# Performance work log

Measured on AMD Instinct MI355X. Metric: run time of the kernel, lower is better.

Reference implementation:

```python
import jax, jax.numpy as jnp
import numpy as np

B, SQ, SV = 2, 2048, 2048
DV, DQ, DK, DO, H = 1024, 1280, 1024, 1024, 16
DHK, DHO = DK // H, DO // H


def setup_inputs() -> dict:
    key = jax.random.key(0)
    ks = jax.random.split(key, 8)
    pre_value_key = jax.random.normal(ks[0], (B, SV, DV), jnp.float32)
    pre_query = jax.random.normal(ks[1], (B, SQ, DQ), jnp.float32)
    value_key_masks = (jax.random.uniform(ks[2], (B, SV)) < 0.9).astype(jnp.float32)
    value_key_counts = jnp.maximum(value_key_masks.sum(-1), 1.0)
    s = 0.02
    Wq = jax.random.normal(ks[3], (DQ, DK), jnp.float32) * s
    bq = jnp.zeros((DK,), jnp.float32)
    Wk = jax.random.normal(ks[4], (DV, DK), jnp.float32) * s
    bk = jnp.zeros((DK,), jnp.float32)
    Wv = jax.random.normal(ks[5], (DV, DO), jnp.float32) * s
    bv = jnp.zeros((DO,), jnp.float32)
    overall_gain = jnp.ones((1, H, 1, 1), jnp.float32)
    overall_bias = jnp.full((1, H, 1, 1), -10.0, jnp.float32)
    return dict(pre_value_key=pre_value_key, pre_query=pre_query,
                value_key_masks=value_key_masks, value_key_counts=value_key_counts,
                Wq=Wq, bq=bq, Wk=Wk, bk=bk, Wv=Wv, bv=bv,
                overall_gain=overall_gain, overall_bias=overall_bias)


def _heads(x, h):
    # (B, S, D) -> (B, h, S, D//h)
    b, s, d = x.shape
    return x.reshape(b, s, h, d // h).transpose(0, 2, 1, 3)


def reference(pre_value_key, pre_query, value_key_masks, value_key_counts,
              Wq, bq, Wk, bk, Wv, bv, overall_gain, overall_bias):
    q = _heads(pre_query @ Wq + bq, H)        # (B,H,SQ,DHK)
    k = _heads(pre_value_key @ Wk + bk, H)    # (B,H,SV,DHK)
    v = _heads(pre_value_key @ Wv + bv, H)    # (B,H,SV,DHO)

    scores = jnp.einsum('bhqd,bhkd->bhqk', q, k) / jnp.sqrt(jnp.float32(DHK))

    mask = value_key_masks  # (B,SV), 0/1 float
    # pooled-score sigmoid gate (cross-attn branch)
    pooled = (scores * mask[:, None, None, :]).sum(-1, keepdims=True)
    pooled = pooled / value_key_counts[:, None, None, None]
    overall_weight = jax.nn.sigmoid(pooled * overall_gain + overall_bias)  # (B,H,SQ,1)

    add_mask = jnp.where(mask == 0, -jnp.inf, 0.0).astype(scores.dtype)
    sm = jax.nn.softmax(scores + add_mask[:, None, None, :], axis=-1)
    h = jnp.einsum('bhqk,bhkd->bhqd', sm, v)  # (B,H,SQ,DHO)

    pq_split = _heads(pre_query[:, :, :DO], H)  # (B,H,SQ,DHO)
    out = pq_split * (1.0 - overall_weight) + h * overall_weight
    out = out.transpose(0, 2, 1, 3).reshape(B, SQ, DO)
    out = jnp.concatenate([out, pre_query[:, :, DO:]], axis=-1)  # (B,SQ,DQ)
    return out
```

## Files before the change

### kernel.cpp

```cpp
#include <hip/hip_runtime.h>

typedef __attribute__((ext_vector_type(8))) __bf16 bf16x8;
typedef __attribute__((ext_vector_type(4))) float f32x4;
typedef __attribute__((ext_vector_type(16))) float f32x16;
typedef __attribute__((ext_vector_type(4))) unsigned short us4;
typedef __attribute__((ext_vector_type(4))) unsigned int u32x4;
typedef __attribute__((address_space(3))) void* as3vp;
typedef const __attribute__((address_space(1))) void* as1vp;

#define GLOAD_LDS16(g, l) __builtin_amdgcn_global_load_lds((as1vp)(g), (as3vp)(l), 16, 0, 0)

#if __has_builtin(__builtin_amdgcn_exp2f)
#define EXP2(x) __builtin_amdgcn_exp2f(x)
#else
#define EXP2(x) __expf((x) * 0.6931471805599453f)
#endif

__device__ __forceinline__ unsigned short f2bf(float f) {
  unsigned u = __builtin_bit_cast(unsigned, f);
  u += 0x7FFFu + ((u >> 16) & 1u);
  return (unsigned short)(u >> 16);
}
__device__ __forceinline__ float bf2f(unsigned short u) {
  return __builtin_bit_cast(float, (unsigned)u << 16);
}
__device__ __forceinline__ unsigned int pkbf(float a, float b) {
  unsigned int r;
  asm("v_cvt_pk_bf16_f32 %0, %1, %2" : "=v"(r) : "v"(a), "v"(b));
  return r;
}

__global__ void prep_all(const float* __restrict__ pre_q, const float* __restrict__ pre_vk,
                         const float* __restrict__ Wq, const float* __restrict__ Wk,
                         const float* __restrict__ Wv, const float* __restrict__ vmask,
                         unsigned short* __restrict__ pq_bf, unsigned short* __restrict__ pv_bf,
                         unsigned short* __restrict__ WqT, unsigned short* __restrict__ WkT,
                         unsigned short* __restrict__ WvT, float* __restrict__ addm,
                         float* __restrict__ km, float* __restrict__ out) {
  __shared__ float tsh[32][33];
  const int bid = blockIdx.x, tid = threadIdx.x;
  if (bid < 5120) {
    const int i = bid * 256 + tid;
    float4 v = ((const float4*)pre_q)[i];
    us4 o;
    o.x = f2bf(v.x); o.y = f2bf(v.y); o.z = f2bf(v.z); o.w = f2bf(v.w);
    ((us4*)pq_bf)[i] = o;
    if ((i % 320) >= 256) ((float4*)out)[i] = v;
  } else if (bid < 9216) {
    const int i = (bid - 5120) * 256 + tid;
    float4 v = ((const float4*)pre_vk)[i];
    us4 o;
    o.x = f2bf(v.x); o.y = f2bf(v.y); o.z = f2bf(v.z); o.w = f2bf(v.w);
    ((us4*)pv_bf)[i] = o;
  } else if (bid < 13056) {
    const int tb = bid - 9216;
    const int z = tb / 1280, rem = tb % 1280;
    const int x = rem & 31, y = rem >> 5;
    const int K = (z == 0) ? 1280 : 1024;
    if (y * 32 >= K) return;
    const float* W = (z == 0) ? Wq : ((z == 1) ? Wk : Wv);
    unsigned short* WT = (z == 0) ? WqT : ((z == 1) ? WkT : WvT);
    const int tx = tid & 31, ty = tid >> 5;
    const int n0 = x * 32, k0 = y * 32;
#pragma unroll
    for (int i = 0; i < 32; i += 8)
      tsh[ty + i][tx] = W[(size_t)(k0 + ty + i) * 1024 + n0 + tx];
    __syncthreads();
#pragma unroll
    for (int i = 0; i < 32; i += 8)
      WT[(size_t)(n0 + ty + i) * K + k0 + tx] = f2bf(tsh[tx][ty + i]);
  } else {
    const int i = (bid - 13056) * 256 + tid;
    addm[i] = (vmask[i] != 0.f) ? 0.f : -1e30f;
    if (i < 2048) km[i] = 0.f;
  }
}

__global__ __launch_bounds__(256, 3)
void gemm_all(const unsigned short* __restrict__ Aq,
              const unsigned short* __restrict__ Akv,
              const unsigned short* __restrict__ WqT,
              const unsigned short* __restrict__ WkT,
              const unsigned short* __restrict__ WvT,
              const float* __restrict__ bq,
              const float* __restrict__ bk,
              const float* __restrict__ bv,
              const float* __restrict__ vmask,
              unsigned short* __restrict__ Qout,
              unsigned short* __restrict__ Kout,
              unsigned short* __restrict__ VFout,
              float* __restrict__ km) {
  __shared__ unsigned short sAB[2][2][128 * 32];
  const int fblk = blockIdx.x;
  const int z = fblk % 3;
  const int rest = fblk / 3;
  const int bx = rest & 31, by = rest >> 5;
  const int KDIM = (z == 0) ? 1280 : 1024;
  const unsigned short* A = (z == 0) ? Aq : Akv;
  const unsigned short* Bt = (z == 0) ? WqT : ((z == 1) ? WkT : WvT);

  const int tid = threadIdx.x, lane = tid & 63, w = tid >> 6;
  const int l15 = lane & 15, lhi = lane >> 4;
  const int wm = w >> 1, wn = w & 1;
  const int row0 = bx * 128, col0 = by * 128;

  const f32x4 zv = {0.f, 0.f, 0.f, 0.f};
  f32x4 acc[4][4];
#pragma unroll
  for (int m = 0; m < 4; ++m)
#pragma unroll
    for (int n = 0; n < 4; ++n) acc[m][n] = zv;

  auto stage = [&](int buf, int kt) {
#pragma unroll
    for (int i = 0; i < 2; ++i) {
      const int c = i * 256 + tid;
      const int r = c >> 2, kc = ((c & 3) ^ (r & 3)) * 8;
      GLOAD_LDS16(A + (size_t)(row0 + r) * KDIM + kt + kc, &sAB[buf][0][0] + c * 8);
      GLOAD_LDS16(Bt + (size_t)(col0 + r) * KDIM + kt + kc, &sAB[buf][1][0] + c * 8);
    }
  };

  const int NT = KDIM / 32;
  stage(0, 0);
  __syncthreads();
  int cur = 0;
  for (int t = 0; t < NT; ++t) {
    if (t + 1 < NT) stage(cur ^ 1, (t + 1) * 32);
    const unsigned short* sAb = &sAB[cur][0][0];
    const unsigned short* sBb = &sAB[cur][1][0];
    const int koS = ((lhi ^ (l15 & 3)) * 8);
    bf16x8 af[4], bfr[4];
#pragma unroll
    for (int m = 0; m < 4; ++m) af[m] = *(const bf16x8*)(sAb + (wm * 64 + m * 16 + l15) * 32 + koS);
#pragma unroll
    for (int n = 0; n < 4; ++n) bfr[n] = *(const bf16x8*)(sBb + (wn * 64 + n * 16 + l15) * 32 + koS);
#pragma unroll
    for (int m = 0; m < 4; ++m)
#pragma unroll
      for (int n = 0; n < 4; ++n)
        acc[m][n] = __builtin_amdgcn_mfma_f32_16x16x32_bf16(af[m], bfr[n], acc[m][n], 0, 0, 0);
    __syncthreads();
    cur ^= 1;
  }

  if (z == 0) {
#pragma unroll
    for (int n = 0; n < 4; ++n) {
      const int gc = col0 + wn * 64 + n * 16 + l15;
      const float bb = bq[gc];
#pragma unroll
      for (int m = 0; m < 4; ++m) {
        const int gr0 = row0 + wm * 64 + m * 16 + lhi * 4;
#pragma unroll
        for (int r = 0; r < 4; ++r)
          Qout[(size_t)(gr0 + r) * 1024 + gc] = f2bf((acc[m][n][r] + bb) * 0.18033688f);
      }
    }
  } else if (z == 1) {
    const int b_ = row0 >> 11;
    const float* maskb = vmask + b_ * 2048;
    f32x4 mv[4];
#pragma unroll
    for (int m = 0; m < 4; ++m)
      mv[m] = *(const f32x4*)(maskb + (row0 & 2047) + wm * 64 + m * 16 + lhi * 4);
#pragma unroll
    for (int n = 0; n < 4; ++n) {
      const int gc = col0 + wn * 64 + n * 16 + l15;
      const float bb = bk[gc];
      float s = 0.f;
#pragma unroll
      for (int m = 0; m < 4; ++m) {
        const int gr0 = row0 + wm * 64 + m * 16 + lhi * 4;
#pragma unroll
        for (int r = 0; r < 4; ++r) {
          const float val = acc[m][n][r] + bb;
          Kout[(size_t)(gr0 + r) * 1024 + gc] = f2bf(val);
          s = fmaf(mv[m][r], val, s);
        }
      }
      s += __shfl_xor(s, 16, 64);
      s += __shfl_xor(s, 32, 64);
      if (lhi == 0) atomicAdd(&km[(b_ * 16 + (gc >> 6)) * 64 + (gc & 63)], s);
    }
  } else {
    __syncthreads();
    unsigned* tb = (unsigned*)&sAB[0][0][0];
#pragma unroll
    for (int n = 0; n < 4; ++n) {
      const int gcL = wn * 64 + n * 16 + l15;
      const float bb = bv[col0 + gcL];
#pragma unroll
      for (int m = 0; m < 4; ++m) {
#pragma unroll
        for (int k = 0; k < 2; ++k) {
          const int grPair = wm * 32 + m * 8 + lhi * 2 + k;
          const int W = (grPair & 3) | ((((grPair >> 2) ^ gcL) & 15) << 2);
          tb[gcL * 64 + W] = pkbf(acc[m][n][2 * k] + bb, acc[m][n][2 * k + 1] + bb);
        }
      }
    }
    __syncthreads();
    const int b_ = row0 >> 11;
#pragma unroll
    for (int it = 0; it < 8; ++it) {
      const int c = it * 256 + tid;
      const int gcL = (c & 63) + ((c >> 10) << 6);
      const int u = (c >> 6) & 15;
      const int W4 = (u ^ gcL) & 15;
      u32x4 o = *(const u32x4*)(tb + gcL * 64 + W4 * 4);
      const int kv0 = (row0 & 2047) + u * 8;
      const int ch = col0 + gcL;
      const int hh2 = ch >> 6, d = ch & 63;
      const int t2 = kv0 >> 6, ks2 = (kv0 >> 4) & 3, h5v = (kv0 >> 3) & 1;
      const size_t off = ((size_t)(b_ * 16 + hh2) << 17) +
                         (size_t)(((t2 * 4 + ks2) * 2 + (d >> 5)) * 64 + h5v * 32 + (d & 31)) * 8;
      *(u32x4*)(VFout + off) = o;
    }
  }
}

__global__ __launch_bounds__(256, 2)
void attn_fused(const unsigned short* __restrict__ Q,
                const unsigned short* __restrict__ Kb,
                const unsigned short* __restrict__ VF,
                const float* __restrict__ addm_g,
                const float* __restrict__ km,
                const float* __restrict__ counts,
                const float* __restrict__ gain,
                const float* __restrict__ gbias,
                const float* __restrict__ pq,
                float* __restrict__ out) {
  __shared__ __align__(16) char smem[32768];
  unsigned short* sK = (unsigned short*)smem;
  float* saddm = (float*)(smem + 16384);
  float* sOT = (float*)smem;

  const int tid = threadIdx.x, lane = tid & 63, w = tid >> 6;
  const int l31 = lane & 31, h5 = lane >> 5;
  const int f = blockIdx.x;
  const int qt = (f >> 3) & 15;
  const int bh = (f & 7) + 8 * (f >> 7);
  const int b = bh >> 4, hh = bh & 15;
  const int q0 = qt * 128;

  GLOAD_LDS16(addm_g + b * 2048 + tid * 4, (char*)saddm + tid * 16);
  GLOAD_LDS16(addm_g + b * 2048 + 1024 + tid * 4, (char*)saddm + 4096 + tid * 16);

  bf16x8 qf[4];
  {
    const unsigned short* qp = Q + (size_t)(b * 2048 + q0 + w * 32 + l31) * 1024 + hh * 64 + h5 * 8;
#pragma unroll
    for (int ks = 0; ks < 4; ++ks) qf[ks] = *(const bf16x8*)(qp + ks * 16);
  }

  float pl_s = 0.f;
  {
    const float* kmp = km + (b * 16 + hh) * 64 + h5 * 8;
#pragma unroll
    for (int ks = 0; ks < 4; ++ks) {
      f32x4 ka = *(const f32x4*)(kmp + ks * 16);
      f32x4 kb4 = *(const f32x4*)(kmp + ks * 16 + 4);
#pragma unroll
      for (int j = 0; j < 4; ++j)
        pl_s += (float)qf[ks][j] * ka[j] + (float)qf[ks][j + 4] * kb4[j];
    }
    float ta = pl_s, tb = pl_s;
    asm("v_permlane32_swap_b32 %0, %1" : "+v"(ta), "+v"(tb));
    pl_s = ta + tb;
  }

  const unsigned short* Kbase = Kb + (size_t)(b * 2048) * 1024 + hh * 64;
  const unsigned short* VFb = VF + ((size_t)bh << 17) + lane * 8;

  f32x16 o0, o1, l_vec;
#pragma unroll
  for (int r = 0; r < 16; ++r) { o0[r] = 0.f; o1[r] = 0.f; l_vec[r] = 0.f; }
  float m_ = -1e30f;

  auto stageK = [&](int buf, int kv) {
#pragma unroll
    for (int i = 0; i < 2; ++i) {
      const int c = i * 256 + tid;
      const int r = c >> 3, sl = (c & 7) ^ (r & 7);
      GLOAD_LDS16(Kbase + (size_t)(kv + r) * 1024 + sl * 8, (char*)sK + buf * 8192 + c * 16);
    }
  };

  bf16x8 vf[8];
  auto ldV = [&](int t) {
    const unsigned short* p = VFb + (size_t)t * 4096;
#pragma unroll
    for (int i = 0; i < 8; ++i) vf[i] = *(const bf16x8*)(p + i * 512);
  };

  stageK(0, 0);
  __syncthreads();
  int cur = 0;

  for (int t = 0; t < 32; ++t) {
    if (t < 31) stageK(cur ^ 1, (t + 1) * 64);
    ldV(t);
    const char* sKc = (const char*)sK + cur * 8192;

    f32x16 s0, s1;
#pragma unroll
    for (int g = 0; g < 4; ++g) {
      f32x4 a0 = *(const f32x4*)(saddm + t * 64 + g * 8 + h5 * 4);
      f32x4 a1 = *(const f32x4*)(saddm + t * 64 + 32 + g * 8 + h5 * 4);
#pragma unroll
      for (int j = 0; j < 4; ++j) { s0[g * 4 + j] = a0[j]; s1[g * 4 + j] = a1[j]; }
    }

#pragma unroll
    for (int ks = 0; ks < 4; ++ks) {
      const int sl = (((ks * 2 + h5) ^ (l31 & 7)) * 16);
      bf16x8 k0 = *(const bf16x8*)(sKc + l31 * 128 + sl);
      bf16x8 k1 = *(const bf16x8*)(sKc + (32 + l31) * 128 + sl);
      s0 = __builtin_amdgcn_mfma_f32_32x32x16_bf16(k0, qf[ks], s0, 0, 0, 0);
      s1 = __builtin_amdgcn_mfma_f32_32x32x16_bf16(k1, qf[ks], s1, 0, 0, 0);
    }

    f32x16 mx;
#pragma unroll
    for (int r = 0; r < 16; ++r) mx[r] = fmaxf(s0[r], s1[r]);
    float t8[8];
#pragma unroll
    for (int r = 0; r < 8; ++r) t8[r] = fmaxf(mx[r], mx[r + 8]);
    float tp = fmaxf(fmaxf(fmaxf(t8[0], t8[1]), fmaxf(t8[2], t8[3])),
                     fmaxf(fmaxf(t8[4], t8[5]), fmaxf(t8[6], t8[7])));
    {
      float ta = tp, tb = tp;
      asm("v_permlane32_swap_b32 %0, %1" : "+v"(ta), "+v"(tb));
      tp = fmaxf(ta, tb);
    }
    if (__any(tp > m_ + 11.0f)) {
      const float mnew = fmaxf(m_, tp);
      const float corr = EXP2(m_ - mnew);
      m_ = mnew;
      l_vec *= corr; o0 *= corr; o1 *= corr;
    }

    f32x16 p0, p1;
#pragma unroll
    for (int r = 0; r < 16; ++r) p0[r] = EXP2(s0[r] - m_);
#pragma unroll
    for (int r = 0; r < 16; ++r) p1[r] = EXP2(s1[r] - m_);
    l_vec += p0; l_vec += p1;

    bf16x8 pfs[4];
    {
      unsigned x0 = pkbf(p0[0], p0[1]), y0 = pkbf(p0[2], p0[3]);
      unsigned z0 = pkbf(p0[4], p0[5]), w0 = pkbf(p0[6], p0[7]);
      asm("v_permlane32_swap_b32 %0, %1" : "+v"(x0), "+v"(z0));
      asm("v_permlane32_swap_b32 %0, %1" : "+v"(y0), "+v"(w0));
      u32x4 f0 = {x0, y0, z0, w0};
      pfs[0] = __builtin_bit_cast(bf16x8, f0);
      unsigned x1 = pkbf(p0[8], p0[9]), y1 = pkbf(p0[10], p0[11]);
      unsigned z1 = pkbf(p0[12], p0[13]), w1 = pkbf(p0[14], p0[15]);
      asm("v_permlane32_swap_b32 %0, %1" : "+v"(x1), "+v"(z1));
      asm("v_permlane32_swap_b32 %0, %1" : "+v"(y1), "+v"(w1));
      u32x4 f1 = {x1, y1, z1, w1};
      pfs[1] = __builtin_bit_cast(bf16x8, f1);
      unsigned x2 = pkbf(p1[0], p1[1]), y2 = pkbf(p1[2], p1[3]);
      unsigned z2 = pkbf(p1[4], p1[5]), w2 = pkbf(p1[6], p1[7]);
      asm("v_permlane32_swap_b32 %0, %1" : "+v"(x2), "+v"(z2));
      asm("v_permlane32_swap_b32 %0, %1" : "+v"(y2), "+v"(w2));
      u32x4 f2 = {x2, y2, z2, w2};
      pfs[2] = __builtin_bit_cast(bf16x8, f2);
      unsigned x3 = pkbf(p1[8], p1[9]), y3 = pkbf(p1[10], p1[11]);
      unsigned z3 = pkbf(p1[12], p1[13]), w3 = pkbf(p1[14], p1[15]);
      asm("v_permlane32_swap_b32 %0, %1" : "+v"(x3), "+v"(z3));
      asm("v_permlane32_swap_b32 %0, %1" : "+v"(y3), "+v"(w3));
      u32x4 f3 = {x3, y3, z3, w3};
      pfs[3] = __builtin_bit_cast(bf16x8, f3);
    }

#pragma unroll
    for (int ks = 0; ks < 4; ++ks) {
      o0 = __builtin_amdgcn_mfma_f32_32x32x16_bf16(vf[ks * 2], pfs[ks], o0, 0, 0, 0);
      o1 = __builtin_amdgcn_mfma_f32_32x32x16_bf16(vf[ks * 2 + 1], pfs[ks], o1, 0, 0, 0);
    }
    __syncthreads();
    cur ^= 1;
  }

  float l_s;
  {
    float a[8];
#pragma unroll
    for (int r = 0; r < 8; ++r) a[r] = l_vec[r] + l_vec[r + 8];
    l_s = ((a[0] + a[1]) + (a[2] + a[3])) + ((a[4] + a[5]) + (a[6] + a[7]));
    float ta = l_s, tb = l_s;
    asm("v_permlane32_swap_b32 %0, %1" : "+v"(ta), "+v"(tb));
    l_s = ta + tb;
  }
  const float po = pl_s * 0.6931471805599453f / counts[b];
  const float wgv = 1.f / (1.f + __expf(-(po * gain[hh] + gbias[hh])));
  const float invl = 1.f / l_s;

  __syncthreads();
  float* myOT = sOT + w * 2048;
#pragma unroll
  for (int r = 0; r < 16; ++r) {
    const int d0 = (r & 3) + 8 * (r >> 2) + 4 * h5;
    myOT[d0 * 32 + (l31 ^ (d0 & 31))] = o0[r] * invl;
    const int d1 = d0 + 32;
    myOT[d1 * 32 + (l31 ^ (d1 & 31))] = o1[r] * invl;
  }
  __syncthreads();
  const size_t rowbase = (size_t)(b * 2048 + q0 + w * 32) * 1280 + hh * 64 + lane;
  const float* pqrow = pq + rowbase;
  float* outrow = out + rowbase;
#pragma unroll 4
  for (int i = 0; i < 32; ++i) {
    const float hval = myOT[lane * 32 + (i ^ (lane & 31))];
    const float wgrow = __shfl(wgv, i, 64);
    const float pv = pqrow[(size_t)i * 1280];
    outrow[(size_t)i * 1280] = fmaf(hval - pv, wgrow, pv);
  }
}

extern "C" void kernel_launch(void* const* d_in, const int* in_sizes, int n_in,
                              void* d_out, int out_size, void* d_ws, size_t ws_size,
                              hipStream_t stream) {
  const float* pre_vk = (const float*)d_in[0];
  const float* pre_q  = (const float*)d_in[1];
  const float* vmask  = (const float*)d_in[2];
  const float* vcnt   = (const float*)d_in[3];
  const float* Wq = (const float*)d_in[4];
  const float* bq = (const float*)d_in[5];
  const float* Wk = (const float*)d_in[6];
  const float* bk = (const float*)d_in[7];
  const float* Wv = (const float*)d_in[8];
  const float* bv = (const float*)d_in[9];
  const float* gain  = (const float*)d_in[10];
  const float* gbias = (const float*)d_in[11];
  float* out = (float*)d_out;

  char* ws = (char*)d_ws;
  unsigned short* pq_bf = (unsigned short*)(ws);
  unsigned short* pv_bf = (unsigned short*)(ws + 10485760);
  unsigned short* WqT   = (unsigned short*)(ws + 18874368);
  unsigned short* WkT   = (unsigned short*)(ws + 21495808);
  unsigned short* WvT   = (unsigned short*)(ws + 23592960);
  unsigned short* Qb    = (unsigned short*)(ws + 25690112);
  unsigned short* Kbb   = (unsigned short*)(ws + 34078720);
  unsigned short* VFb   = (unsigned short*)(ws + 42467328);
  float*          kmb   = (float*)(ws + 50855936);
  float*          addm  = (float*)(ws + 50864128);

  prep_all<<<13072, 256, 0, stream>>>(pre_q, pre_vk, Wq, Wk, Wv, vmask,
                                      pq_bf, pv_bf, WqT, WkT, WvT, addm, kmb, out);
  gemm_all<<<768, 256, 0, stream>>>(pq_bf, pv_bf, WqT, WkT, WvT, bq, bk, bv, vmask,
                                    Qb, Kbb, VFb, kmb);
  attn_fused<<<512, 256, 0, stream>>>(Qb, Kbb, VFb, addm, kmb, vcnt, gain, gbias, pre_q, out);
}
```

Measured before the change: 106.9 us.

## Process two KV tiles per iteration with split softmax states and MFMA priority

The attention loop now handles 128 keys per iteration as two independent 64-key streams, each with its own running max, denominator and output accumulators, merged once at the end. K staging doubles to 16KB per buffer, so fewer barriers run, and the two independent chains give the scheduler more MFMA/softmax work to interleave. s_setprio is raised around MFMA sections. The cost is much higher register pressure from the duplicated accumulators and V fragments, which could spill or hurt occupancy under launch_bounds(256,2), plus more LDS.

```diff
diff --git a/kernel.cpp b/kernel.cpp
--- a/kernel.cpp
+++ b/kernel.cpp
@@ -231,9 +231,9 @@
                 const float* __restrict__ gbias,
                 const float* __restrict__ pq,
                 float* __restrict__ out) {
-  __shared__ __align__(16) char smem[32768];
+  __shared__ __align__(16) char smem[40960];
   unsigned short* sK = (unsigned short*)smem;
-  float* saddm = (float*)(smem + 16384);
+  float* saddm = (float*)(smem + 32768);
   float* sOT = (float*)smem;
 
   const int tid = threadIdx.x, lane = tid & 63, w = tid >> 6;
@@ -273,140 +273,203 @@
   const unsigned short* Kbase = Kb + (size_t)(b * 2048) * 1024 + hh * 64;
   const unsigned short* VFb = VF + ((size_t)bh << 17) + lane * 8;
 
-  f32x16 o0, o1, l_vec;
-#pragma unroll
-  for (int r = 0; r < 16; ++r) { o0[r] = 0.f; o1[r] = 0.f; l_vec[r] = 0.f; }
-  float m_ = -1e30f;
+  f32x16 oA0, oA1, oB0, oB1, lA, lB;
+#pragma unroll
+  for (int r = 0; r < 16; ++r) {
+    oA0[r] = 0.f; oA1[r] = 0.f; oB0[r] = 0.f; oB1[r] = 0.f;
+    lA[r] = 0.f; lB[r] = 0.f;
+  }
+  float mA = -1e30f, mB = -1e30f;
 
   auto stageK = [&](int buf, int kv) {
 #pragma unroll
-    for (int i = 0; i < 2; ++i) {
+    for (int i = 0; i < 4; ++i) {
       const int c = i * 256 + tid;
       const int r = c >> 3, sl = (c & 7) ^ (r & 7);
-      GLOAD_LDS16(Kbase + (size_t)(kv + r) * 1024 + sl * 8, (char*)sK + buf * 8192 + c * 16);
+      GLOAD_LDS16(Kbase + (size_t)(kv + r) * 1024 + sl * 8, (char*)sK + buf * 16384 + c * 16);
     }
   };
 
-  bf16x8 vf[8];
-  auto ldV = [&](int t) {
+  auto ldV = [&](int t, bf16x8 (&vv)[8]) {
     const unsigned short* p = VFb + (size_t)t * 4096;
 #pragma unroll
-    for (int i = 0; i < 8; ++i) vf[i] = *(const bf16x8*)(p + i * 512);
+    for (int i = 0; i < 8; ++i) vv[i] = *(const bf16x8*)(p + i * 512);
+  };
+
+  auto mkpfs = [&](const f32x16& p0, const f32x16& p1, bf16x8 (&pfs)[4]) {
+    unsigned x0 = pkbf(p0[0], p0[1]), y0 = pkbf(p0[2], p0[3]);
+    unsigned z0 = pkbf(p0[4], p0[5]), w0 = pkbf(p0[6], p0[7]);
+    asm("v_permlane32_swap_b32 %0, %1" : "+v"(x0), "+v"(z0));
+    asm("v_permlane32_swap_b32 %0, %1" : "+v"(y0), "+v"(w0));
+    u32x4 f0 = {x0, y0, z0, w0};
+    pfs[0] = __builtin_bit_cast(bf16x8, f0);
+    unsigned x1 = pkbf(p0[8], p0[9]), y1 = pkbf(p0[10], p0[11]);
+    unsigned z1 = pkbf(p0[12], p0[13]), w1 = pkbf(p0[14], p0[15]);
+    asm("v_permlane32_swap_b32 %0, %1" : "+v"(x1), "+v"(z1));
+    asm("v_permlane32_swap_b32 %0, %1" : "+v"(y1), "+v"(w1));
+    u32x4 f1 = {x1, y1, z1, w1};
+    pfs[1] = __builtin_bit_cast(bf16x8, f1);
+    unsigned x2 = pkbf(p1[0], p1[1]), y2 = pkbf(p1[2], p1[3]);
+    unsigned z2 = pkbf(p1[4], p1[5]), w2 = pkbf(p1[6], p1[7]);
+    asm("v_permlane32_swap_b32 %0, %1" : "+v"(x2), "+v"(z2));
+    asm("v_permlane32_swap_b32 %0, %1" : "+v"(y2), "+v"(w2));
+    u32x4 f2 = {x2, y2, z2, w2};
+    pfs[2] = __builtin_bit_cast(bf16x8, f2);
+    unsigned x3 = pkbf(p1[8], p1[9]), y3 = pkbf(p1[10], p1[11]);
+    unsigned z3 = pkbf(p1[12], p1[13]), w3 = pkbf(p1[14], p1[15]);
+    asm("v_permlane32_swap_b32 %0, %1" : "+v"(x3), "+v"(z3));
+    asm("v_permlane32_swap_b32 %0, %1" : "+v"(y3), "+v"(w3));
+    u32x4 f3 = {x3, y3, z3, w3};
+    pfs[3] = __builtin_bit_cast(bf16x8, f3);
   };
 
   stageK(0, 0);
   __syncthreads();
   int cur = 0;
 
-  for (int t = 0; t < 32; ++t) {
-    if (t < 31) stageK(cur ^ 1, (t + 1) * 64);
-    ldV(t);
-    const char* sKc = (const char*)sK + cur * 8192;
-
-    f32x16 s0, s1;
+  for (int T = 0; T < 16; ++T) {
+    if (T < 15) stageK(cur ^ 1, (T + 1) * 128);
+    bf16x8 vfa[8], vfb[8];
+    ldV(2 * T, vfa);
+    ldV(2 * T + 1, vfb);
+    const char* sKc = (const char*)sK + cur * 16384;
+
+    f32x16 s0a, s1a, s0b, s1b;
 #pragma unroll
     for (int g = 0; g < 4; ++g) {
-      f32x4 a0 = *(const f32x4*)(saddm + t * 64 + g * 8 + h5 * 4);
-      f32x4 a1 = *(const f32x4*)(saddm + t * 64 + 32 + g * 8 + h5 * 4);
-#pragma unroll
-      for (int j = 0; j < 4; ++j) { s0[g * 4 + j] = a0[j]; s1[g * 4 + j] = a1[j]; }
-    }
-
+      f32x4 a0 = *(const f32x4*)(saddm + T * 128 + g * 8 + h5 * 4);
+      f32x4 a1 = *(const f32x4*)(saddm + T * 128 + 32 + g * 8 + h5 * 4);
+      f32x4 b0 = *(const f32x4*)(saddm + T * 128 + 64 + g * 8 + h5 * 4);
+      f32x4 b1 = *(const f32x4*)(saddm + T * 128 + 96 + g * 8 + h5 * 4);
+#pragma unroll
+      for (int j = 0; j < 4; ++j) {
+        s0a[g * 4 + j] = a0[j]; s1a[g * 4 + j] = a1[j];
+        s0b[g * 4 + j] = b0[j]; s1b[g * 4 + j] = b1[j];
+      }
+    }
+
+    __builtin_amdgcn_s_setprio(1);
 #pragma unroll
     for (int ks = 0; ks < 4; ++ks) {
       const int sl = (((ks * 2 + h5) ^ (l31 & 7)) * 16);
-      bf16x8 k0 = *(const bf16x8*)(sKc + l31 * 128 + sl);
-      bf16x8 k1 = *(const bf16x8*)(sKc + (32 + l31) * 128 + sl);
-      s0 = __builtin_amdgcn_mfma_f32_32x32x16_bf16(k0, qf[ks], s0, 0, 0, 0);
-      s1 = __builtin_amdgcn_mfma_f32_32x32x16_bf16(k1, qf[ks], s1, 0, 0, 0);
-    }
-
-    f32x16 mx;
-#pragma unroll
-    for (int r = 0; r < 16; ++r) mx[r] = fmaxf(s0[r], s1[r]);
-    float t8[8];
-#pragma unroll
-    for (int r = 0; r < 8; ++r) t8[r] = fmaxf(mx[r], mx[r + 8]);
-    float tp = fmaxf(fmaxf(fmaxf(t8[0], t8[1]), fmaxf(t8[2], t8[3])),
-                     fmaxf(fmaxf(t8[4], t8[5]), fmaxf(t8[6], t8[7])));
+      bf16x8 k0a = *(const bf16x8*)(sKc + l31 * 128 + sl);
+      bf16x8 k1a = *(const bf16x8*)(sKc + (32 + l31) * 128 + sl);
+      bf16x8 k0b = *(const bf16x8*)(sKc + (64 + l31) * 128 + sl);
+      bf16x8 k1b = *(const bf16x8*)(sKc + (96 + l31) * 128 + sl);
+      s0a = __builtin_amdgcn_mfma_f32_32x32x16_bf16(k0a, qf[ks], s0a, 0, 0, 0);
+      s1a = __builtin_amdgcn_mfma_f32_32x32x16_bf16(k1a, qf[ks], s1a, 0, 0, 0);
+      s0b = __builtin_amdgcn_mfma_f32_32x32x16_bf16(k0b, qf[ks], s0b, 0, 0, 0);
+      s1b = __builtin_amdgcn_mfma_f32_32x32x16_bf16(k1b, qf[ks], s1b, 0, 0, 0);
+    }
+    __builtin_amdgcn_s_setprio(0);
+
     {
+      f32x16 mx;
+#pragma unroll
+      for (int r = 0; r < 16; ++r) mx[r] = fmaxf(s0a[r], s1a[r]);
+      float t8[8];
+#pragma unroll
+      for (int r = 0; r < 8; ++r) t8[r] = fmaxf(mx[r], mx[r + 8]);
+      float tp = fmaxf(fmaxf(fmaxf(t8[0], t8[1]), fmaxf(t8[2], t8[3])),
+                       fmaxf(fmaxf(t8[4], t8[5]), fmaxf(t8[6], t8[7])));
       float ta = tp, tb = tp;
       asm("v_permlane32_swap_b32 %0, %1" : "+v"(ta), "+v"(tb));
       tp = fmaxf(ta, tb);
-    }
-    if (__any(tp > m_ + 11.0f)) {
-      const float mnew = fmaxf(m_, tp);
-      const float corr = EXP2(m_ - mnew);
-      m_ = mnew;
-      l_vec *= corr; o0 *= corr; o1 *= corr;
-    }
-
-    f32x16 p0, p1;
-#pragma unroll
-    for (int r = 0; r < 16; ++r) p0[r] = EXP2(s0[r] - m_);
-#pragma unroll
-    for (int r = 0; r < 16; ++r) p1[r] = EXP2(s1[r] - m_);
-    l_vec += p0; l_vec += p1;
-
-    bf16x8 pfs[4];
+      if (__any(tp > mA + 11.0f)) {
+        const float mnew = fmaxf(mA, tp);
+        const float corr = EXP2(mA - mnew);
+        mA = mnew;
+        lA *= corr; oA0 *= corr; oA1 *= corr;
+      }
+      f32x16 p0, p1;
+#pragma unroll
+      for (int r = 0; r < 16; ++r) p0[r] = EXP2(s0a[r] - mA);
+#pragma unroll
+      for (int r = 0; r < 16; ++r) p1[r] = EXP2(s1a[r] - mA);
+      lA += p0; lA += p1;
+      bf16x8 pfs[4];
+      mkpfs(p0, p1, pfs);
+      __builtin_amdgcn_s_setprio(1);
+#pragma unroll
+      for (int ks = 0; ks < 4; ++ks) {
+        oA0 = __builtin_amdgcn_mfma_f32_32x32x16_bf16(vfa[ks * 2], pfs[ks], oA0, 0, 0, 0);
+        oA1 = __builtin_amdgcn_mfma_f32_32x32x16_bf16(vfa[ks * 2 + 1], pfs[ks], oA1, 0, 0, 0);
+      }
+      __builtin_amdgcn_s_setprio(0);
+    }
+
     {
-      unsigned x0 = pkbf(p0[0], p0[1]), y0 = pkbf(p0[2], p0[3]);
-      unsigned z0 = pkbf(p0[4], p0[5]), w0 = pkbf(p0[6], p0[7]);
-      asm("v_permlane32_swap_b32 %0, %1" : "+v"(x0), "+v"(z0));
-      asm("v_permlane32_swap_b32 %0, %1" : "+v"(y0), "+v"(w0));
-      u32x4 f0 = {x0, y0, z0, w0};
-      pfs[0] = __builtin_bit_cast(bf16x8, f0);
-      unsigned x1 = pkbf(p0[8], p0[9]), y1 = pkbf(p0[10], p0[11]);
-      unsigned z1 = pkbf(p0[12], p0[13]), w1 = pkbf(p0[14], p0[15]);
-      asm("v_permlane32_swap_b32 %0, %1" : "+v"(x1), "+v"(z1));
-      asm("v_permlane32_swap_b32 %0, %1" : "+v"(y1), "+v"(w1));
-      u32x4 f1 = {x1, y1, z1, w1};
-      pfs[1] = __builtin_bit_cast(bf16x8, f1);
-      unsigned x2 = pkbf(p1[0], p1[1]), y2 = pkbf(p1[2], p1[3]);
-      unsigned z2 = pkbf(p1[4], p1[5]), w2 = pkbf(p1[6], p1[7]);
-      asm("v_permlane32_swap_b32 %0, %1" : "+v"(x2), "+v"(z2));
-      asm("v_permlane32_swap_b32 %0, %1" : "+v"(y2), "+v"(w2));
-      u32x4 f2 = {x2, y2, z2, w2};
-      pfs[2] = __builtin_bit_cast(bf16x8, f2);
-      unsigned x3 = pkbf(p1[8], p1[9]), y3 = pkbf(p1[10], p1[11]);
-      unsigned z3 = pkbf(p1[12], p1[13]), w3 = pkbf(p1[14], p1[15]);
-      asm("v_permlane32_swap_b32 %0, %1" : "+v"(x3), "+v"(z3));
-      asm("v_permlane32_swap_b32 %0, %1" : "+v"(y3), "+v"(w3));
-      u32x4 f3 = {x3, y3, z3, w3};
-      pfs[3] = __builtin_bit_cast(bf16x8, f3);
-    }
-
-#pragma unroll
-    for (int ks = 0; ks < 4; ++ks) {
-      o0 = __builtin_amdgcn_mfma_f32_32x32x16_bf16(vf[ks * 2], pfs[ks], o0, 0, 0, 0);
-      o1 = __builtin_amdgcn_mfma_f32_32x32x16_bf16(vf[ks * 2 + 1], pfs[ks], o1, 0, 0, 0);
-    }
+      f32x16 mx;
+#pragma unroll
+      for (int r = 0; r < 16; ++r) mx[r] = fmaxf(s0b[r], s1b[r]);
+      float t8[8];
+#pragma unroll
+      for (int r = 0; r < 8; ++r) t8[r] = fmaxf(mx[r], mx[r + 8]);
+      float tp = fmaxf(fmaxf(fmaxf(t8[0], t8[1]), fmaxf(t8[2], t8[3])),
+                       fmaxf(fmaxf(t8[4], t8[5]), fmaxf(t8[6], t8[7])));
+      float ta = tp, tb = tp;
+      asm("v_permlane32_swap_b32 %0, %1" : "+v"(ta), "+v"(tb));
+      tp = fmaxf(ta, tb);
+      if (__any(tp > mB + 11.0f)) {
+        const float mnew = fmaxf(mB, tp);
+        const float corr = EXP2(mB - mnew);
+        mB = mnew;
+        lB *= corr; oB0 *= corr; oB1 *= corr;
+      }
+      f32x16 p0, p1;
+#pragma unroll
+      for (int r = 0; r < 16; ++r) p0[r] = EXP2(s0b[r] - mB);
+#pragma unroll
+      for (int r = 0; r < 16; ++r) p1[r] = EXP2(s1b[r] - mB);
+      lB += p0; lB += p1;
+      bf16x8 pfs[4];
+      mkpfs(p0, p1, pfs);
+      __builtin_amdgcn_s_setprio(1);
+#pragma unroll
+      for (int ks = 0; ks < 4; ++ks) {
+        oB0 = __builtin_amdgcn_mfma_f32_32x32x16_bf16(vfb[ks * 2], pfs[ks], oB0, 0, 0, 0);
+        oB1 = __builtin_amdgcn_mfma_f32_32x32x16_bf16(vfb[ks * 2 + 1], pfs[ks], oB1, 0, 0, 0);
+      }
+      __builtin_amdgcn_s_setprio(0);
+    }
+
     __syncthreads();
     cur ^= 1;
   }
 
-  float l_s;
+  float lA_s, lB_s;
   {
     float a[8];
 #pragma unroll
-    for (int r = 0; r < 8; ++r) a[r] = l_vec[r] + l_vec[r + 8];
-    l_s = ((a[0] + a[1]) + (a[2] + a[3])) + ((a[4] + a[5]) + (a[6] + a[7]));
-    float ta = l_s, tb = l_s;
+    for (int r = 0; r < 8; ++r) a[r] = lA[r] + lA[r + 8];
+    lA_s = ((a[0] + a[1]) + (a[2] + a[3])) + ((a[4] + a[5]) + (a[6] + a[7]));
+    float ta = lA_s, tb = lA_s;
     asm("v_permlane32_swap_b32 %0, %1" : "+v"(ta), "+v"(tb));
-    l_s = ta + tb;
-  }
+    lA_s = ta + tb;
+#pragma unroll
+    for (int r = 0; r < 8; ++r) a[r] = lB[r] + lB[r + 8];
+    lB_s = ((a[0] + a[1]) + (a[2] + a[3])) + ((a[4] + a[5]) + (a[6] + a[7]));
+    float tc = lB_s, td = lB_s;
+    asm("v_permlane32_swap_b32 %0, %1" : "+v"(tc), "+v"(td));
+    lB_s = tc + td;
+  }
+  const float mM = fmaxf(mA, mB);
+  const float scA = EXP2(mA - mM), scB = EXP2(mB - mM);
+  const float l_s = lA_s * scA + lB_s * scB;
+  const float invl = 1.f / l_s;
+  const float sA_ = scA * invl, sB_ = scB * invl;
+
   const float po = pl_s * 0.6931471805599453f / counts[b];
   const float wgv = 1.f / (1.f + __expf(-(po * gain[hh] + gbias[hh])));
-  const float invl = 1.f / l_s;
 
   __syncthreads();
   float* myOT = sOT + w * 2048;
 #pragma unroll
   for (int r = 0; r < 16; ++r) {
     const int d0 = (r & 3) + 8 * (r >> 2) + 4 * h5;
-    myOT[d0 * 32 + (l31 ^ (d0 & 31))] = o0[r] * invl;
+    myOT[d0 * 32 + (l31 ^ (d0 & 31))] = oA0[r] * sA_ + oB0[r] * sB_;
     const int d1 = d0 + 32;
-    myOT[d1 * 32 + (l31 ^ (d1 & 31))] = o1[r] * invl;
+    myOT[d1 * 32 + (l31 ^ (d1 & 31))] = oA1[r] * sA_ + oB1[r] * sB_;
   }
   __syncthreads();
   const size_t rowbase = (size_t)(b * 2048 + q0 + w * 32) * 1280 + hh * 64 + lane;
```

After: 129.4 us. 1.21x slower.
